# Kernel tuning notes

Measured on AMD Instinct MI355X. Metric: run time of the kernel, lower is better.

The kernel has to match this reference:

```python
import jax, jax.numpy as jnp
import numpy as np

H1, W1GRID, K_SIZE, B = 28, 28, 5, 512
K2 = K_SIZE * K_SIZE  # 25 kernel weight matrices
_BITS = np.array([[0, 0], [0, 1], [1, 0], [1, 1]])  # 2^dim basis combos


def _grid_edges(h, w):
    """8-neighborhood grid graph; returns (src, dst, pseudo in [0,1]^2)."""
    ys, xs = np.meshgrid(np.arange(h), np.arange(w), indexing='ij')
    node = (ys * w + xs).reshape(-1)
    ys, xs = ys.reshape(-1), xs.reshape(-1)
    srcs, dsts, pses = [], [], []
    for dy in (-1, 0, 1):
        for dx in (-1, 0, 1):
            if dy == 0 and dx == 0:
                continue
            ny, nx = ys + dy, xs + dx
            ok = (ny >= 0) & (ny < h) & (nx >= 0) & (nx < w)
            srcs.append((ny * w + nx)[ok])   # neighbor j
            dsts.append(node[ok])            # center i
            p = np.array([[(dx + 1) / 2.0, (dy + 1) / 2.0]], dtype=np.float32)
            pses.append(np.repeat(p, ok.sum(), axis=0))
    return (np.concatenate(srcs), np.concatenate(dsts), np.concatenate(pses))


def _batched_graph(h, w, batch):
    s, d, p = _grid_edges(h, w)
    n = h * w
    off = (np.arange(batch, dtype=np.int64) * n)[:, None]
    src = (s[None, :] + off).reshape(-1)
    dst = (d[None, :] + off).reshape(-1)
    pse = np.tile(p, (batch, 1))
    return np.stack([src, dst]), pse


def setup_inputs() -> dict:
    key = jax.random.key(0)
    ks = jax.random.split(key, 8)
    e1, p1 = _batched_graph(28, 28, B)
    e2, p2 = _batched_graph(14, 14, B)
    return {
        'x': jax.random.uniform(ks[0], (B * 784, 1), jnp.float32),
        'pseudo1': jnp.asarray(p1), 'pseudo2': jnp.asarray(p2),
        'W1': jax.random.normal(ks[1], (K2, 1, 32), jnp.float32) * 0.2,
        'root1': jax.random.normal(ks[2], (1, 32), jnp.float32) * 0.2,
        'b1': jnp.zeros((32,), jnp.float32),
        'W2': jax.random.normal(ks[3], (K2, 32, 64), jnp.float32) * 0.05,
        'root2': jax.random.normal(ks[4], (32, 64), jnp.float32) * 0.05,
        'b2': jnp.zeros((64,), jnp.float32),
        'fc1_w': jax.random.normal(ks[5], (3136, 512), jnp.float32) * 0.02,
        'fc1_b': jnp.zeros((512,), jnp.float32),
        'fc2_w': jax.random.normal(ks[6], (512, 10), jnp.float32) * 0.05,
        'fc2_b': jnp.zeros((10,), jnp.float32),
        'edge_index1': jnp.asarray(e1, jnp.int64 if jax.config.jax_enable_x64 else jnp.int32),
        'edge_index2': jnp.asarray(e2, jnp.int64 if jax.config.jax_enable_x64 else jnp.int32),
    }


def _spline_basis(pseudo, k):
    # open B-spline, degree 1: each dim contributes 2 knots with linear weights
    frac = pseudo * (k - 1)                                   # [E,2]
    lo = jnp.clip(jnp.floor(frac), 0, k - 2)
    f = frac - lo                                             # [E,2]
    w = jnp.stack([1.0 - f, f], axis=-1)                      # [E,2,2]
    idx = jnp.stack([lo, lo + 1], axis=-1).astype(jnp.int32)  # [E,2,2]
    basis = w[:, 0, _BITS[:, 0]] * w[:, 1, _BITS[:, 1]]       # [E,4]
    widx = idx[:, 0, _BITS[:, 0]] + idx[:, 1, _BITS[:, 1]] * k  # [E,4]
    return basis, widx


def _spline_conv(x, edge_index, pseudo, W, root, bias, n_nodes, k):
    src, dst = edge_index[0], edge_index[1]
    x_j = x[src]                                              # [E,Cin] gather
    basis, widx = _spline_basis(pseudo, k)                    # [E,4]
    kk = k * k
    flat = (dst[:, None] * kk + widx).reshape(-1)             # [E*4]
    contrib = (basis[:, :, None] * x_j[:, None, :]).reshape(-1, x.shape[1])
    S = jnp.zeros((n_nodes * kk, x.shape[1]), x.dtype).at[flat].add(contrib)
    S = S.reshape(n_nodes, kk, x.shape[1])                    # per-node per-kernel sums
    deg = jnp.zeros((n_nodes,), x.dtype).at[dst].add(1.0)
    out = jnp.einsum('nki,kio->no', S, W) / jnp.maximum(deg, 1.0)[:, None]
    return out + x @ root + bias


def _pool2x2(x, b, hw, c):
    return x.reshape(b, hw // 2, 2, hw // 2, 2, c).max(axis=(2, 4))


def reference(x, pseudo1, pseudo2, W1, root1, b1, W2, root2, b2,
              fc1_w, fc1_b, fc2_w, fc2_b, edge_index1, edge_index2):
    n1 = x.shape[0]
    b = n1 // 784
    h = jax.nn.elu(_spline_conv(x, edge_index1, pseudo1, W1, root1, b1, n1, K_SIZE))
    h = _pool2x2(h, b, 28, 32).reshape(-1, 32)                # [B*196,32]
    h = jax.nn.elu(_spline_conv(h, edge_index2, pseudo2, W2, root2, b2, b * 196, K_SIZE))
    h = _pool2x2(h, b, 14, 64).reshape(-1, 7 * 7 * 64)        # [B,3136]
    h = jax.nn.elu(h @ fc1_w + fc1_b)
    # dropout is identity in eval mode
    h = jax.nn.elu(h @ fc2_w + fc2_b)
    return jax.nn.log_softmax(h, axis=-1)
```

## Files before the change

### kernel.cpp

```cpp
#include <hip/hip_runtime.h>
#include <math.h>

#define BATCH 512

__device__ __forceinline__ float elu1(float v) {
    return v > 0.f ? v : expm1f(v);
}
__device__ __forceinline__ float4 elu4(float4 v) {
    return make_float4(elu1(v.x), elu1(v.y), elu1(v.z), elu1(v.w));
}

__global__ __launch_bounds__(256) void k1_conv1_pool(
    const float* __restrict__ x, const float* __restrict__ W1,
    const float* __restrict__ root1, const float* __restrict__ b1,
    float* __restrict__ p1) {
    __shared__ float xs[900];
    __shared__ float w1s[8 * 32 + 64];
    const int b = blockIdx.x;
    const int t = threadIdx.x;

    for (int l = t; l < 900; l += 256) xs[l] = 0.f;
    {
        int d = t >> 5, c = t & 31;
        int e = d + (d >= 4 ? 1 : 0);
        int dy = e / 3 - 1, dx = e % 3 - 1;
        int widx = 2 * (dx + 1) + 10 * (dy + 1);
        w1s[t] = W1[widx * 32 + c];
        if (t < 32) { w1s[256 + t] = root1[t]; w1s[288 + t] = b1[t]; }
    }
    __syncthreads();
    const float* xb = x + (size_t)b * 784;
    for (int l = t; l < 784; l += 256) {
        int y = l / 28, xx = l % 28;
        xs[(y + 1) * 30 + xx + 1] = xb[l];
    }
    __syncthreads();

    if (t >= 196) return;
    int py = t / 14, px = t % 14;
    int xbse[4];
    float xc[4], inv[4];
    #pragma unroll
    for (int p = 0; p < 4; ++p) {
        int sy = p >> 1, sx = p & 1;
        int y = 2 * py + sy, xx = 2 * px + sx;
        xbse[p] = (y + 1) * 30 + xx + 1;
        xc[p] = xs[xbse[p]];
        int nvy = 3 - (y == 0) - (y == 27);
        int nvx = 3 - (xx == 0) - (xx == 27);
        inv[p] = 1.f / (float)(nvy * nvx - 1);
    }
    const float4* w4 = (const float4*)w1s;
    float* outp = p1 + ((size_t)b * 196 + t) * 32;

    #pragma unroll
    for (int h = 0; h < 2; ++h) {
        float4 acc[4][4];
        #pragma unroll
        for (int p = 0; p < 4; ++p)
            #pragma unroll
            for (int q = 0; q < 4; ++q) acc[p][q] = make_float4(0.f, 0.f, 0.f, 0.f);
        #pragma unroll
        for (int d = 0; d < 8; ++d) {
            int e = d + (d >= 4 ? 1 : 0);
            int od = (e / 3 - 1) * 30 + (e % 3 - 1);
            float4 w0 = w4[d * 8 + h * 4 + 0];
            float4 w1 = w4[d * 8 + h * 4 + 1];
            float4 w2 = w4[d * 8 + h * 4 + 2];
            float4 w3 = w4[d * 8 + h * 4 + 3];
            #pragma unroll
            for (int p = 0; p < 4; ++p) {
                float xv = xs[xbse[p] + od];
                acc[p][0].x += xv * w0.x; acc[p][0].y += xv * w0.y; acc[p][0].z += xv * w0.z; acc[p][0].w += xv * w0.w;
                acc[p][1].x += xv * w1.x; acc[p][1].y += xv * w1.y; acc[p][1].z += xv * w1.z; acc[p][1].w += xv * w1.w;
                acc[p][2].x += xv * w2.x; acc[p][2].y += xv * w2.y; acc[p][2].z += xv * w2.z; acc[p][2].w += xv * w2.w;
                acc[p][3].x += xv * w3.x; acc[p][3].y += xv * w3.y; acc[p][3].z += xv * w3.z; acc[p][3].w += xv * w3.w;
            }
        }
        #pragma unroll
        for (int q = 0; q < 4; ++q) {
            float4 rt = w4[64 + h * 4 + q];
            float4 bs = w4[72 + h * 4 + q];
            float4 m = make_float4(-1e30f, -1e30f, -1e30f, -1e30f);
            #pragma unroll
            for (int p = 0; p < 4; ++p) {
                float4 v;
                v.x = elu1(acc[p][q].x * inv[p] + xc[p] * rt.x + bs.x);
                v.y = elu1(acc[p][q].y * inv[p] + xc[p] * rt.y + bs.y);
                v.z = elu1(acc[p][q].z * inv[p] + xc[p] * rt.z + bs.z);
                v.w = elu1(acc[p][q].w * inv[p] + xc[p] * rt.w + bs.w);
                m.x = fmaxf(m.x, v.x); m.y = fmaxf(m.y, v.y);
                m.z = fmaxf(m.z, v.z); m.w = fmaxf(m.w, v.w);
            }
            *(float4*)(outp + h * 16 + q * 4) = m;
        }
    }
}

__global__ __launch_bounds__(256) void k2_conv2_pool(
    const float* __restrict__ p1, const float* __restrict__ W2,
    const float* __restrict__ root2, const float* __restrict__ b2,
    float* __restrict__ p2) {
    __shared__ float xs[8448];
    __shared__ float wb[2][2048];
    const int b = blockIdx.x;
    const int t = threadIdx.x;
    const int cell = t >> 2, cg = t & 3;

    {
        const float4* s4 = (const float4*)W2;
        float4* w4p = (float4*)wb[0];
        w4p[t] = s4[t]; w4p[t + 256] = s4[t + 256];
    }
    for (int l = t; l < 8448; l += 256) xs[l] = 0.f;
    __syncthreads();
    {
        const float* src = p1 + (size_t)b * 6272;
        for (int l = t; l < 6272; l += 256) {
            int node = l >> 5, i = l & 31;
            int y = node / 14, xx = node - y * 14;
            xs[((y + 1) * 16 + xx + 1) * 33 + i] = src[l];
        }
    }
    __syncthreads();

    const int ccell = (cell < 49) ? cell : 48;
    const int py = ccell / 7, px = ccell - py * 7;
    int nb[4];
    float inv[4];
    #pragma unroll
    for (int p = 0; p < 4; ++p) {
        int sy = p >> 1, sx = p & 1;
        int y = 2 * py + sy, xx = 2 * px + sx;
        nb[p] = ((y + 1) * 16 + xx + 1) * 33;
        int nvy = 3 - (y == 0) - (y == 13);
        int nvx = 3 - (xx == 0) - (xx == 13);
        inv[p] = 1.f / (float)(nvy * nvx - 1);
    }

    float4 acc[4][4];
    #pragma unroll
    for (int p = 0; p < 4; ++p)
        #pragma unroll
        for (int q = 0; q < 4; ++q) acc[p][q] = make_float4(0.f, 0.f, 0.f, 0.f);

    for (int d = 0; d < 9; ++d) {
        float4 pf0, pf1;
        if (d < 8) {
            int nd = d + 1;
            const float* nsrc;
            if (nd == 8) nsrc = root2;
            else {
                int e = nd + (nd >= 4 ? 1 : 0);
                int dy = e / 3 - 1, dx = e % 3 - 1;
                nsrc = W2 + (size_t)(2 * (dx + 1) + 10 * (dy + 1)) * 2048;
            }
            pf0 = ((const float4*)nsrc)[t];
            pf1 = ((const float4*)nsrc)[t + 256];
        }
        if (d == 8) {
            #pragma unroll
            for (int p = 0; p < 4; ++p) {
                acc[p][0].x *= inv[p]; acc[p][0].y *= inv[p]; acc[p][0].z *= inv[p]; acc[p][0].w *= inv[p];
                acc[p][1].x *= inv[p]; acc[p][1].y *= inv[p]; acc[p][1].z *= inv[p]; acc[p][1].w *= inv[p];
                acc[p][2].x *= inv[p]; acc[p][2].y *= inv[p]; acc[p][2].z *= inv[p]; acc[p][2].w *= inv[p];
                acc[p][3].x *= inv[p]; acc[p][3].y *= inv[p]; acc[p][3].z *= inv[p]; acc[p][3].w *= inv[p];
            }
        }
        int od33 = 0;
        if (d < 8) {
            int e = d + (d >= 4 ? 1 : 0);
            od33 = ((e / 3 - 1) * 16 + (e % 3 - 1)) * 33;
        }
        const float* wcur = wb[d & 1] + cg * 16;
        const float* xc0 = xs + nb[0] + od33;
        const float* xc1 = xs + nb[1] + od33;
        const float* xc2 = xs + nb[2] + od33;
        const float* xc3 = xs + nb[3] + od33;
        #pragma unroll 2
        for (int i = 0; i < 32; ++i) {
            float4 w0 = *(const float4*)(wcur + i * 64 + 0);
            float4 w1 = *(const float4*)(wcur + i * 64 + 4);
            float4 w2 = *(const float4*)(wcur + i * 64 + 8);
            float4 w3 = *(const float4*)(wcur + i * 64 + 12);
            float x0 = xc0[i], x1 = xc1[i], x2 = xc2[i], x3 = xc3[i];
            acc[0][0].x += x0 * w0.x; acc[0][0].y += x0 * w0.y; acc[0][0].z += x0 * w0.z; acc[0][0].w += x0 * w0.w;
            acc[0][1].x += x0 * w1.x; acc[0][1].y += x0 * w1.y; acc[0][1].z += x0 * w1.z; acc[0][1].w += x0 * w1.w;
            acc[0][2].x += x0 * w2.x; acc[0][2].y += x0 * w2.y; acc[0][2].z += x0 * w2.z; acc[0][2].w += x0 * w2.w;
            acc[0][3].x += x0 * w3.x; acc[0][3].y += x0 * w3.y; acc[0][3].z += x0 * w3.z; acc[0][3].w += x0 * w3.w;
            acc[1][0].x += x1 * w0.x; acc[1][0].y += x1 * w0.y; acc[1][0].z += x1 * w0.z; acc[1][0].w += x1 * w0.w;
            acc[1][1].x += x1 * w1.x; acc[1][1].y += x1 * w1.y; acc[1][1].z += x1 * w1.z; acc[1][1].w += x1 * w1.w;
            acc[1][2].x += x1 * w2.x; acc[1][2].y += x1 * w2.y; acc[1][2].z += x1 * w2.z; acc[1][2].w += x1 * w2.w;
            acc[1][3].x += x1 * w3.x; acc[1][3].y += x1 * w3.y; acc[1][3].z += x1 * w3.z; acc[1][3].w += x1 * w3.w;
            acc[2][0].x += x2 * w0.x; acc[2][0].y += x2 * w0.y; acc[2][0].z += x2 * w0.z; acc[2][0].w += x2 * w0.w;
            acc[2][1].x += x2 * w1.x; acc[2][1].y += x2 * w1.y; acc[2][1].z += x2 * w1.z; acc[2][1].w += x2 * w1.w;
            acc[2][2].x += x2 * w2.x; acc[2][2].y += x2 * w2.y; acc[2][2].z += x2 * w2.z; acc[2][2].w += x2 * w2.w;
            acc[2][3].x += x2 * w3.x; acc[2][3].y += x2 * w3.y; acc[2][3].z += x2 * w3.z; acc[2][3].w += x2 * w3.w;
            acc[3][0].x += x3 * w0.x; acc[3][0].y += x3 * w0.y; acc[3][0].z += x3 * w0.z; acc[3][0].w += x3 * w0.w;
            acc[3][1].x += x3 * w1.x; acc[3][1].y += x3 * w1.y; acc[3][1].z += x3 * w1.z; acc[3][1].w += x3 * w1.w;
            acc[3][2].x += x3 * w2.x; acc[3][2].y += x3 * w2.y; acc[3][2].z += x3 * w2.z; acc[3][2].w += x3 * w2.w;
            acc[3][3].x += x3 * w3.x; acc[3][3].y += x3 * w3.y; acc[3][3].z += x3 * w3.z; acc[3][3].w += x3 * w3.w;
        }
        if (d < 8) {
            float4* wn = (float4*)wb[(d + 1) & 1];
            wn[t] = pf0; wn[t + 256] = pf1;
        }
        __syncthreads();
    }

    if (cell < 49) {
        float* outp = p2 + (size_t)b * 3136 + cell * 64 + cg * 16;
        #pragma unroll
        for (int q = 0; q < 4; ++q) {
            float4 bs = *(const float4*)(b2 + cg * 16 + q * 4);
            float4 m = make_float4(-1e30f, -1e30f, -1e30f, -1e30f);
            #pragma unroll
            for (int p = 0; p < 4; ++p) {
                float4 v;
                v.x = elu1(acc[p][q].x + bs.x);
                v.y = elu1(acc[p][q].y + bs.y);
                v.z = elu1(acc[p][q].z + bs.z);
                v.w = elu1(acc[p][q].w + bs.w);
                m.x = fmaxf(m.x, v.x); m.y = fmaxf(m.y, v.y);
                m.z = fmaxf(m.z, v.z); m.w = fmaxf(m.w, v.w);
            }
            *(float4*)(outp + q * 4) = m;
        }
    }
}

__global__ __launch_bounds__(256) void k3a_fc1(
    const float* __restrict__ A, const float* __restrict__ B,
    float* __restrict__ part) {
    __shared__ float As[16 * 64];
    __shared__ float Bs[16 * 64];
    const int t = threadIdx.x;
    const int tx = t & 15, ty = t >> 4;
    const int n0 = blockIdx.x * 64, m0 = blockIdx.y * 64, kz = blockIdx.z;
    const int nchunk = (kz < 4) ? 25 : 24;
    const int c0 = (kz < 4) ? kz * 25 : 100 + (kz - 4) * 24;

    const float* Abase = A + (size_t)m0 * 3136 + c0 * 16;
    const float* Bbase = B + (size_t)c0 * 16 * 512 + n0;

    float4 accr[4];
    #pragma unroll
    for (int r = 0; r < 4; ++r) accr[r] = make_float4(0.f, 0.f, 0.f, 0.f);

    const int ma = t >> 2, kqa = t & 3;
    const int kb = t >> 4, n4 = t & 15;

    for (int kk = 0; kk < nchunk; ++kk) {
        float4 av = *(const float4*)(Abase + (size_t)ma * 3136 + kk * 16 + kqa * 4);
        float4 bv = *(const float4*)(Bbase + (size_t)(kk * 16 + kb) * 512 + n4 * 4);
        As[(kqa * 4 + 0) * 64 + ma] = av.x;
        As[(kqa * 4 + 1) * 64 + ma] = av.y;
        As[(kqa * 4 + 2) * 64 + ma] = av.z;
        As[(kqa * 4 + 3) * 64 + ma] = av.w;
        *(float4*)&Bs[kb * 64 + n4 * 4] = bv;
        __syncthreads();
        #pragma unroll
        for (int k = 0; k < 16; ++k) {
            float4 a4 = *(const float4*)&As[k * 64 + ty * 4];
            float4 b4 = *(const float4*)&Bs[k * 64 + tx * 4];
            accr[0].x += a4.x * b4.x; accr[0].y += a4.x * b4.y; accr[0].z += a4.x * b4.z; accr[0].w += a4.x * b4.w;
            accr[1].x += a4.y * b4.x; accr[1].y += a4.y * b4.y; accr[1].z += a4.y * b4.z; accr[1].w += a4.y * b4.w;
            accr[2].x += a4.z * b4.x; accr[2].y += a4.z * b4.y; accr[2].z += a4.z * b4.z; accr[2].w += a4.z * b4.w;
            accr[3].x += a4.w * b4.x; accr[3].y += a4.w * b4.y; accr[3].z += a4.w * b4.z; accr[3].w += a4.w * b4.w;
        }
        __syncthreads();
    }
    #pragma unroll
    for (int r = 0; r < 4; ++r)
        *(float4*)(part + ((size_t)kz * 512 + m0 + ty * 4 + r) * 512 + n0 + tx * 4) = accr[r];
}

__global__ __launch_bounds__(256) void k3b_reduce(
    const float* __restrict__ part, const float* __restrict__ bias,
    float* __restrict__ h3) {
    int gid = blockIdx.x * 256 + threadIdx.x;
    const float4* p4 = (const float4*)part;
    float4 s = make_float4(0.f, 0.f, 0.f, 0.f);
    #pragma unroll
    for (int kz = 0; kz < 8; ++kz) {
        float4 v = p4[(size_t)kz * 65536 + gid];
        s.x += v.x; s.y += v.y; s.z += v.z; s.w += v.w;
    }
    float4 b4 = *(const float4*)(bias + (gid & 127) * 4);
    s.x += b4.x; s.y += b4.y; s.z += b4.z; s.w += b4.w;
    ((float4*)h3)[gid] = elu4(s);
}

__global__ __launch_bounds__(256) void k4_fc2_lsm(
    const float* __restrict__ h, const float* __restrict__ w,
    const float* __restrict__ bias, float* __restrict__ out) {
    const int t = threadIdx.x, lane = t & 63;
    const int wv = (blockIdx.x * 256 + t) >> 6;
    float wl[8][10];
    #pragma unroll
    for (int j = 0; j < 8; ++j)
        #pragma unroll
        for (int o = 0; o < 10; ++o) wl[j][o] = w[(lane + 64 * j) * 10 + o];
    float bo[10];
    #pragma unroll
    for (int o = 0; o < 10; ++o) bo[o] = bias[o];

    for (int row = wv; row < 512; row += 64) {
        float acc[10];
        #pragma unroll
        for (int o = 0; o < 10; ++o) acc[o] = 0.f;
        #pragma unroll
        for (int j = 0; j < 8; ++j) {
            float hv = h[(size_t)row * 512 + lane + 64 * j];
            #pragma unroll
            for (int o = 0; o < 10; ++o) acc[o] += hv * wl[j][o];
        }
        #pragma unroll
        for (int s = 32; s; s >>= 1)
            #pragma unroll
            for (int o = 0; o < 10; ++o) acc[o] += __shfl_xor(acc[o], s, 64);
        float v[10], m = -1e30f;
        #pragma unroll
        for (int o = 0; o < 10; ++o) { v[o] = elu1(acc[o] + bo[o]); m = fmaxf(m, v[o]); }
        float ssum = 0.f;
        #pragma unroll
        for (int o = 0; o < 10; ++o) ssum += expf(v[o] - m);
        float lse = m + logf(ssum);
        if (lane < 10) {
            float val = v[0];
            #pragma unroll
            for (int o = 1; o < 10; ++o) val = (lane == o) ? v[o] : val;
            out[(size_t)row * 10 + lane] = val - lse;
        }
    }
}

extern "C" void kernel_launch(void* const* d_in, const int* in_sizes, int n_in,
                              void* d_out, int out_size, void* d_ws, size_t ws_size,
                              hipStream_t stream) {
    const float* x     = (const float*)d_in[0];
    const float* W1    = (const float*)d_in[3];
    const float* root1 = (const float*)d_in[4];
    const float* b1v   = (const float*)d_in[5];
    const float* W2    = (const float*)d_in[6];
    const float* root2 = (const float*)d_in[7];
    const float* b2v   = (const float*)d_in[8];
    const float* fc1w  = (const float*)d_in[9];
    const float* fc1b  = (const float*)d_in[10];
    const float* fc2w  = (const float*)d_in[11];
    const float* fc2b  = (const float*)d_in[12];

    float* ws = (float*)d_ws;
    float* p1 = ws;
    float* p2 = p1 + (size_t)BATCH * 196 * 32;
    float* h3 = p2 + (size_t)BATCH * 49 * 64;
    float* part = p1;

    k1_conv1_pool<<<dim3(BATCH), 256, 0, stream>>>(x, W1, root1, b1v, p1);
    k2_conv2_pool<<<dim3(BATCH), 256, 0, stream>>>(p1, W2, root2, b2v, p2);
    k3a_fc1<<<dim3(8, 8, 8), 256, 0, stream>>>(p2, fc1w, part);
    k3b_reduce<<<dim3(256), 256, 0, stream>>>(part, fc1b, h3);
    k4_fc2_lsm<<<dim3(16), 256, 0, stream>>>(h3, fc2w, fc2b, (float*)d_out);
}
```

Measured before the change: 137.7 us.

## Pad conv2 weight smem, retile fc1 GEMM with double buffering, fuse reduce+fc2

```diff
diff --git a/kernel.cpp b/kernel.cpp
--- a/kernel.cpp
+++ b/kernel.cpp
@@ -5,9 +5,6 @@
 
 __device__ __forceinline__ float elu1(float v) {
     return v > 0.f ? v : expm1f(v);
-}
-__device__ __forceinline__ float4 elu4(float4 v) {
-    return make_float4(elu1(v.x), elu1(v.y), elu1(v.z), elu1(v.w));
 }
 
 __global__ __launch_bounds__(256) void k1_conv1_pool(
@@ -102,15 +99,21 @@
     const float* __restrict__ root2, const float* __restrict__ b2,
     float* __restrict__ p2) {
     __shared__ float xs[8448];
-    __shared__ float wb[2][2048];
+    __shared__ float wb[2][2176];
     const int b = blockIdx.x;
     const int t = threadIdx.x;
     const int cell = t >> 2, cg = t & 3;
+    const int coff = cg * 16 + (cg >> 1) * 4;
 
     {
         const float4* s4 = (const float4*)W2;
         float4* w4p = (float4*)wb[0];
-        w4p[t] = s4[t]; w4p[t + 256] = s4[t + 256];
+        #pragma unroll
+        for (int j = 0; j < 2; ++j) {
+            int l = t + j * 256;
+            int i = l >> 4, c4 = l & 15, g = c4 >> 2, q = c4 & 3;
+            w4p[i * 17 + g * 4 + (g >> 1) + q] = s4[l];
+        }
     }
     for (int l = t; l < 8448; l += 256) xs[l] = 0.f;
     __syncthreads();
@@ -172,17 +175,17 @@
             int e = d + (d >= 4 ? 1 : 0);
             od33 = ((e / 3 - 1) * 16 + (e % 3 - 1)) * 33;
         }
-        const float* wcur = wb[d & 1] + cg * 16;
+        const float* wcur = wb[d & 1] + coff;
         const float* xc0 = xs + nb[0] + od33;
         const float* xc1 = xs + nb[1] + od33;
         const float* xc2 = xs + nb[2] + od33;
         const float* xc3 = xs + nb[3] + od33;
         #pragma unroll 2
         for (int i = 0; i < 32; ++i) {
-            float4 w0 = *(const float4*)(wcur + i * 64 + 0);
-            float4 w1 = *(const float4*)(wcur + i * 64 + 4);
-            float4 w2 = *(const float4*)(wcur + i * 64 + 8);
-            float4 w3 = *(const float4*)(wcur + i * 64 + 12);
+            float4 w0 = *(const float4*)(wcur + i * 68 + 0);
+            float4 w1 = *(const float4*)(wcur + i * 68 + 4);
+            float4 w2 = *(const float4*)(wcur + i * 68 + 8);
+            float4 w3 = *(const float4*)(wcur + i * 68 + 12);
             float x0 = xc0[i], x1 = xc1[i], x2 = xc2[i], x3 = xc3[i];
             acc[0][0].x += x0 * w0.x; acc[0][0].y += x0 * w0.y; acc[0][0].z += x0 * w0.z; acc[0][0].w += x0 * w0.w;
             acc[0][1].x += x0 * w1.x; acc[0][1].y += x0 * w1.y; acc[0][1].z += x0 * w1.z; acc[0][1].w += x0 * w1.w;
@@ -203,7 +206,12 @@
         }
         if (d < 8) {
             float4* wn = (float4*)wb[(d + 1) & 1];
-            wn[t] = pf0; wn[t + 256] = pf1;
+            #pragma unroll
+            for (int j = 0; j < 2; ++j) {
+                int l = t + j * 256;
+                int i = l >> 4, c4 = l & 15, g = c4 >> 2, q = c4 & 3;
+                wn[i * 17 + g * 4 + (g >> 1) + q] = (j == 0) ? pf0 : pf1;
+            }
         }
         __syncthreads();
     }
@@ -231,107 +239,127 @@
 
 __global__ __launch_bounds__(256) void k3a_fc1(
     const float* __restrict__ A, const float* __restrict__ B,
-    float* __restrict__ part) {
-    __shared__ float As[16 * 64];
-    __shared__ float Bs[16 * 64];
+    float* __restrict__ part, int kchunk) {
+    __shared__ float As[2][16][128];
+    __shared__ float Bs[2][16][132];
     const int t = threadIdx.x;
     const int tx = t & 15, ty = t >> 4;
-    const int n0 = blockIdx.x * 64, m0 = blockIdx.y * 64, kz = blockIdx.z;
-    const int nchunk = (kz < 4) ? 25 : 24;
-    const int c0 = (kz < 4) ? kz * 25 : 100 + (kz - 4) * 24;
-
-    const float* Abase = A + (size_t)m0 * 3136 + c0 * 16;
-    const float* Bbase = B + (size_t)c0 * 16 * 512 + n0;
-
-    float4 accr[4];
-    #pragma unroll
-    for (int r = 0; r < 4; ++r) accr[r] = make_float4(0.f, 0.f, 0.f, 0.f);
-
-    const int ma = t >> 2, kqa = t & 3;
-    const int kb = t >> 4, n4 = t & 15;
-
-    for (int kk = 0; kk < nchunk; ++kk) {
-        float4 av = *(const float4*)(Abase + (size_t)ma * 3136 + kk * 16 + kqa * 4);
-        float4 bv = *(const float4*)(Bbase + (size_t)(kk * 16 + kb) * 512 + n4 * 4);
-        As[(kqa * 4 + 0) * 64 + ma] = av.x;
-        As[(kqa * 4 + 1) * 64 + ma] = av.y;
-        As[(kqa * 4 + 2) * 64 + ma] = av.z;
-        As[(kqa * 4 + 3) * 64 + ma] = av.w;
-        *(float4*)&Bs[kb * 64 + n4 * 4] = bv;
+    const int n0 = blockIdx.x * 128, m0 = blockIdx.y * 128;
+    const int k0 = blockIdx.z * kchunk;
+    const int steps = kchunk >> 4;
+
+    const int sm = t & 127, skh = t >> 7;
+    const int sk = t >> 4, snq = t & 15;
+    const float* Ap = A + (size_t)(m0 + sm) * 3136 + k0 + skh * 8;
+    const float* Bp = B + (size_t)(k0 + sk) * 512 + n0 + snq * 8;
+
+    {
+        float4 a0 = *(const float4*)Ap;
+        float4 a1 = *(const float4*)(Ap + 4);
+        float4 b0 = *(const float4*)Bp;
+        float4 b1 = *(const float4*)(Bp + 4);
+        As[0][skh * 8 + 0][sm] = a0.x; As[0][skh * 8 + 1][sm] = a0.y;
+        As[0][skh * 8 + 2][sm] = a0.z; As[0][skh * 8 + 3][sm] = a0.w;
+        As[0][skh * 8 + 4][sm] = a1.x; As[0][skh * 8 + 5][sm] = a1.y;
+        As[0][skh * 8 + 6][sm] = a1.z; As[0][skh * 8 + 7][sm] = a1.w;
+        *(float4*)&Bs[0][sk][snq * 8] = b0;
+        *(float4*)&Bs[0][sk][snq * 8 + 4] = b1;
+    }
+    __syncthreads();
+
+    float acc[8][8];
+    #pragma unroll
+    for (int r = 0; r < 8; ++r)
+        #pragma unroll
+        for (int c = 0; c < 8; ++c) acc[r][c] = 0.f;
+
+    for (int s = 0; s < steps; ++s) {
+        float4 a0, a1, b0, b1;
+        if (s + 1 < steps) {
+            a0 = *(const float4*)(Ap + (s + 1) * 16);
+            a1 = *(const float4*)(Ap + (s + 1) * 16 + 4);
+            b0 = *(const float4*)(Bp + (size_t)(s + 1) * 16 * 512);
+            b1 = *(const float4*)(Bp + (size_t)(s + 1) * 16 * 512 + 4);
+        }
+        const int cur = s & 1;
+        #pragma unroll
+        for (int k = 0; k < 16; ++k) {
+            float4 av0 = *(const float4*)&As[cur][k][ty * 8];
+            float4 av1 = *(const float4*)&As[cur][k][ty * 8 + 4];
+            float4 bv0 = *(const float4*)&Bs[cur][k][tx * 4];
+            float4 bv1 = *(const float4*)&Bs[cur][k][64 + tx * 4];
+            float ar[8] = {av0.x, av0.y, av0.z, av0.w, av1.x, av1.y, av1.z, av1.w};
+            #pragma unroll
+            for (int r = 0; r < 8; ++r) {
+                acc[r][0] += ar[r] * bv0.x; acc[r][1] += ar[r] * bv0.y;
+                acc[r][2] += ar[r] * bv0.z; acc[r][3] += ar[r] * bv0.w;
+                acc[r][4] += ar[r] * bv1.x; acc[r][5] += ar[r] * bv1.y;
+                acc[r][6] += ar[r] * bv1.z; acc[r][7] += ar[r] * bv1.w;
+            }
+        }
+        if (s + 1 < steps) {
+            const int nxt = cur ^ 1;
+            As[nxt][skh * 8 + 0][sm] = a0.x; As[nxt][skh * 8 + 1][sm] = a0.y;
+            As[nxt][skh * 8 + 2][sm] = a0.z; As[nxt][skh * 8 + 3][sm] = a0.w;
+            As[nxt][skh * 8 + 4][sm] = a1.x; As[nxt][skh * 8 + 5][sm] = a1.y;
+            As[nxt][skh * 8 + 6][sm] = a1.z; As[nxt][skh * 8 + 7][sm] = a1.w;
+            *(float4*)&Bs[nxt][sk][snq * 8] = b0;
+            *(float4*)&Bs[nxt][sk][snq * 8 + 4] = b1;
+        }
         __syncthreads();
-        #pragma unroll
-        for (int k = 0; k < 16; ++k) {
-            float4 a4 = *(const float4*)&As[k * 64 + ty * 4];
-            float4 b4 = *(const float4*)&Bs[k * 64 + tx * 4];
-            accr[0].x += a4.x * b4.x; accr[0].y += a4.x * b4.y; accr[0].z += a4.x * b4.z; accr[0].w += a4.x * b4.w;
-            accr[1].x += a4.y * b4.x; accr[1].y += a4.y * b4.y; accr[1].z += a4.y * b4.z; accr[1].w += a4.y * b4.w;
-            accr[2].x += a4.z * b4.x; accr[2].y += a4.z * b4.y; accr[2].z += a4.z * b4.z; accr[2].w += a4.z * b4.w;
-            accr[3].x += a4.w * b4.x; accr[3].y += a4.w * b4.y; accr[3].z += a4.w * b4.z; accr[3].w += a4.w * b4.w;
-        }
-        __syncthreads();
-    }
-    #pragma unroll
-    for (int r = 0; r < 4; ++r)
-        *(float4*)(part + ((size_t)kz * 512 + m0 + ty * 4 + r) * 512 + n0 + tx * 4) = accr[r];
-}
-
-__global__ __launch_bounds__(256) void k3b_reduce(
-    const float* __restrict__ part, const float* __restrict__ bias,
-    float* __restrict__ h3) {
-    int gid = blockIdx.x * 256 + threadIdx.x;
-    const float4* p4 = (const float4*)part;
-    float4 s = make_float4(0.f, 0.f, 0.f, 0.f);
-    #pragma unroll
-    for (int kz = 0; kz < 8; ++kz) {
-        float4 v = p4[(size_t)kz * 65536 + gid];
-        s.x += v.x; s.y += v.y; s.z += v.z; s.w += v.w;
-    }
-    float4 b4 = *(const float4*)(bias + (gid & 127) * 4);
-    s.x += b4.x; s.y += b4.y; s.z += b4.z; s.w += b4.w;
-    ((float4*)h3)[gid] = elu4(s);
-}
-
-__global__ __launch_bounds__(256) void k4_fc2_lsm(
-    const float* __restrict__ h, const float* __restrict__ w,
-    const float* __restrict__ bias, float* __restrict__ out) {
-    const int t = threadIdx.x, lane = t & 63;
-    const int wv = (blockIdx.x * 256 + t) >> 6;
-    float wl[8][10];
-    #pragma unroll
-    for (int j = 0; j < 8; ++j)
-        #pragma unroll
-        for (int o = 0; o < 10; ++o) wl[j][o] = w[(lane + 64 * j) * 10 + o];
-    float bo[10];
-    #pragma unroll
-    for (int o = 0; o < 10; ++o) bo[o] = bias[o];
-
-    for (int row = wv; row < 512; row += 64) {
-        float acc[10];
-        #pragma unroll
-        for (int o = 0; o < 10; ++o) acc[o] = 0.f;
-        #pragma unroll
-        for (int j = 0; j < 8; ++j) {
-            float hv = h[(size_t)row * 512 + lane + 64 * j];
-            #pragma unroll
-            for (int o = 0; o < 10; ++o) acc[o] += hv * wl[j][o];
-        }
-        #pragma unroll
-        for (int s = 32; s; s >>= 1)
-            #pragma unroll
-            for (int o = 0; o < 10; ++o) acc[o] += __shfl_xor(acc[o], s, 64);
+    }
+
+    float* pbase = part + ((size_t)blockIdx.z * 512 + m0 + ty * 8) * 512 + n0;
+    #pragma unroll
+    for (int r = 0; r < 8; ++r) {
+        float4 o0 = make_float4(acc[r][0], acc[r][1], acc[r][2], acc[r][3]);
+        float4 o1 = make_float4(acc[r][4], acc[r][5], acc[r][6], acc[r][7]);
+        *(float4*)(pbase + (size_t)r * 512 + tx * 4) = o0;
+        *(float4*)(pbase + (size_t)r * 512 + 64 + tx * 4) = o1;
+    }
+}
+
+__global__ __launch_bounds__(256) void k34_reduce_fc2_lsm(
+    const float* __restrict__ part, const float* __restrict__ fc1b,
+    const float* __restrict__ w, const float* __restrict__ fc2b,
+    float* __restrict__ out, int KZ) {
+    __shared__ float red[4][10];
+    const int b = blockIdx.x, t = threadIdx.x;
+
+    float a0 = fc1b[t], a1 = fc1b[t + 256];
+    for (int kz = 0; kz < KZ; ++kz) {
+        const float* pr = part + ((size_t)kz * 512 + b) * 512;
+        a0 += pr[t]; a1 += pr[t + 256];
+    }
+    a0 = elu1(a0); a1 = elu1(a1);
+
+    float acc[10];
+    #pragma unroll
+    for (int o = 0; o < 10; ++o)
+        acc[o] = a0 * w[t * 10 + o] + a1 * w[(t + 256) * 10 + o];
+    #pragma unroll
+    for (int s = 32; s; s >>= 1)
+        #pragma unroll
+        for (int o = 0; o < 10; ++o) acc[o] += __shfl_xor(acc[o], s, 64);
+    if ((t & 63) == 0) {
+        #pragma unroll
+        for (int o = 0; o < 10; ++o) red[t >> 6][o] = acc[o];
+    }
+    __syncthreads();
+    if (t == 0) {
         float v[10], m = -1e30f;
         #pragma unroll
-        for (int o = 0; o < 10; ++o) { v[o] = elu1(acc[o] + bo[o]); m = fmaxf(m, v[o]); }
+        for (int o = 0; o < 10; ++o) {
+            float s = red[0][o] + red[1][o] + red[2][o] + red[3][o] + fc2b[o];
+            v[o] = elu1(s);
+            m = fmaxf(m, v[o]);
+        }
         float ssum = 0.f;
         #pragma unroll
         for (int o = 0; o < 10; ++o) ssum += expf(v[o] - m);
         float lse = m + logf(ssum);
-        if (lane < 10) {
-            float val = v[0];
-            #pragma unroll
-            for (int o = 1; o < 10; ++o) val = (lane == o) ? v[o] : val;
-            out[(size_t)row * 10 + lane] = val - lse;
-        }
+        #pragma unroll
+        for (int o = 0; o < 10; ++o) out[(size_t)b * 10 + o] = v[o] - lse;
     }
 }
 
@@ -353,12 +381,17 @@
     float* ws = (float*)d_ws;
     float* p1 = ws;
     float* p2 = p1 + (size_t)BATCH * 196 * 32;
-    float* h3 = p2 + (size_t)BATCH * 49 * 64;
-    float* part = p1;
+    float* tail = p2 + (size_t)BATCH * 49 * 64;
+
+    const size_t base_f = 3211264u + 1605632u;
+    int KZ; float* part;
+    if (ws_size >= (base_f + 28u * 262144u) * 4u)      { KZ = 28; part = tail; }
+    else if (ws_size >= (base_f + 14u * 262144u) * 4u) { KZ = 14; part = tail; }
+    else                                               { KZ = 7;  part = p1; }
+    const int kchunk = 3136 / KZ;
 
     k1_conv1_pool<<<dim3(BATCH), 256, 0, stream>>>(x, W1, root1, b1v, p1);
     k2_conv2_pool<<<dim3(BATCH), 256, 0, stream>>>(p1, W2, root2, b2v, p2);
-    k3a_fc1<<<dim3(8, 8, 8), 256, 0, stream>>>(p2, fc1w, part);
-    k3b_reduce<<<dim3(256), 256, 0, stream>>>(part, fc1b, h3);
-    k4_fc2_lsm<<<dim3(16), 256, 0, stream>>>(h3, fc2w, fc2b, (float*)d_out);
-}
+    k3a_fc1<<<dim3(4, 4, KZ), 256, 0, stream>>>(p2, fc1w, part, kchunk);
+    k34_reduce_fc2_lsm<<<dim3(BATCH), 256, 0, stream>>>(part, fc1b, fc2w, fc2b, (float*)d_out, KZ);
+}
```

Result: faster. 132.6 us (-3.7%).
